# Kernel optimization log

Measured on AMD Instinct MI355X. Metric: run time of the kernel, lower is better.

Reference implementation:

```python
import jax, jax.numpy as jnp
import numpy as np

B, S, D, H = 2, 2048, 1024, 16
DH = D // H  # per-head depth = 64


def setup_inputs() -> dict:
    key = jax.random.key(0)
    ks = jax.random.split(key, 10)
    s = 1.0 / np.sqrt(D)
    return {
        "q_in": jax.random.normal(ks[0], (B, S, D), jnp.float32),
        "k_in": jax.random.normal(ks[1], (B, S, D), jnp.float32),
        "v_in": jax.random.normal(ks[2], (B, S, D), jnp.float32),
        "mask": jnp.zeros((B, 1, S, S), jnp.float32),
        "Wq": jax.random.normal(ks[3], (D, D), jnp.float32) * s,
        "bq": jnp.zeros((D,), jnp.float32),
        "Wk": jax.random.normal(ks[4], (D, D), jnp.float32) * s,
        "bk": jnp.zeros((D,), jnp.float32),
        "Wv": jax.random.normal(ks[5], (D, D), jnp.float32) * s,
        "bv": jnp.zeros((D,), jnp.float32),
        "Wo": jax.random.normal(ks[6], (D, D), jnp.float32) * s,
        "bo": jnp.zeros((D,), jnp.float32),
    }


def _split_heads(x):
    # [B,S,D] -> [B,H,S,DH]
    b, s, _ = x.shape
    return x.reshape(b, s, H, DH).transpose(0, 2, 1, 3)


def reference(q_in, k_in, v_in, mask, Wq, bq, Wk, bk, Wv, bv, Wo, bo):
    q = _split_heads(q_in @ Wq + bq)
    k = _split_heads(k_in @ Wk + bk)
    v = _split_heads(v_in @ Wv + bv)
    logits = jnp.einsum("bhqd,bhkd->bhqk", q, k) / jnp.sqrt(jnp.float32(DH))
    logits = logits + mask * -1e9
    attn = jax.nn.softmax(logits, axis=-1)
    ctx = jnp.einsum("bhqk,bhkd->bhqd", attn, v)  # [B,H,S,DH]
    concat = ctx.transpose(0, 2, 1, 3).reshape(q_in.shape[0], -1, D)
    out = concat @ Wo + bo  # dropout is identity at inference
    return out, attn
```

## Files before the change

### kernel.cpp

```cpp
#include <hip/hip_runtime.h>
#include <hip/hip_bf16.h>

static constexpr int cB = 2, cS = 2048, cD = 1024, cH = 16, cDH = 64;

typedef __attribute__((ext_vector_type(4))) float f32x4;
typedef __attribute__((ext_vector_type(8))) short s16x8;
typedef unsigned long long u64;
typedef unsigned short u16;

__device__ inline f32x4 mfma16(s16x8 a, s16x8 b, f32x4 c) {
  return __builtin_amdgcn_mfma_f32_16x16x32_bf16(a, b, c, 0, 0, 0);
}

__device__ inline u16 f2bf(float x) {
  unsigned u = __float_as_uint(x);
  u += 0x7FFFu + ((u >> 16) & 1u);
  return (u16)(u >> 16);
}

__device__ inline unsigned cvt_pk_bf16(float lo, float hi) {
  unsigned r;
  asm("v_cvt_pk_bf16_f32 %0, %1, %2" : "=v"(r) : "v"(lo), "v"(hi));
  return r;
}

__device__ inline f32x4 zero4() { f32x4 z; z[0] = z[1] = z[2] = z[3] = 0.f; return z; }

__device__ inline void gload16(const void* src, void* dst) {
  __builtin_amdgcn_global_load_lds((const __attribute__((address_space(1))) void*)src,
                                   (__attribute__((address_space(3))) void*)dst, 16, 0, 0);
}

__global__ __launch_bounds__(256) void wt4_kernel(const float* __restrict__ W0,
                                                  const float* __restrict__ W1,
                                                  const float* __restrict__ W2,
                                                  const float* __restrict__ W3,
                                                  u16* __restrict__ T0, u16* __restrict__ T1,
                                                  u16* __restrict__ T2, u16* __restrict__ T3) {
  __shared__ float tile[32][33];
  int z = blockIdx.z;
  const float* W = z == 0 ? W0 : z == 1 ? W1 : z == 2 ? W2 : W3;
  u16* Wt = z == 0 ? T0 : z == 1 ? T1 : z == 2 ? T2 : T3;
  int tx = threadIdx.x, ty = threadIdx.y;
  int r0 = blockIdx.y * 32, c0 = blockIdx.x * 32;
  for (int i = ty; i < 32; i += 8)
    tile[i][tx] = W[(size_t)(r0 + i) * cD + c0 + tx];
  __syncthreads();
  for (int i = ty; i < 32; i += 8)
    Wt[(size_t)(c0 + i) * cD + r0 + tx] = f2bf(tile[tx][i]);
}

__global__ __launch_bounds__(256) void maskflag_kernel(const float* __restrict__ mask,
                                                       unsigned char* __restrict__ flags) {
  int blk = blockIdx.x;
  int b = blk >> 10, qt = (blk >> 5) & 31, kt = blk & 31;
  int t = threadIdx.x;
  int r = t >> 2, c0 = (t & 3) * 16;
  const float4* p = (const float4*)(mask + ((size_t)b * cS + qt * 64 + r) * cS + kt * 64 + c0);
  int any = 0;
  for (int j = 0; j < 4; ++j) {
    float4 v = p[j];
    any |= (v.x != 0.f) | (v.y != 0.f) | (v.z != 0.f) | (v.w != 0.f);
  }
  __shared__ int sred;
  if (t == 0) sred = 0;
  __syncthreads();
  if (any) atomicOr(&sred, 1);
  __syncthreads();
  if (t == 0) flags[blk] = (unsigned char)sred;
}

template<bool AFP32, bool OUTF32>
__global__ __launch_bounds__(256) void gemm128(const void* __restrict__ Ap,
                                               const u16* __restrict__ Bt,
                                               const float* __restrict__ bias,
                                               void* __restrict__ outp,
                                               float scale, int vt_mode) {
  __shared__ __attribute__((aligned(16))) u16 As[128 * 64];
  __shared__ __attribute__((aligned(16))) u16 Bs[128 * 64];
  int t = threadIdx.x;
  int w = t >> 6, l = t & 63, g = l >> 4, li = l & 15;
  int bm = blockIdx.x & 31, bn = blockIdx.x >> 5;
  int m0 = bm * 128, n0 = bn * 128;
  int wr = w >> 1, wc = w & 1;

  f32x4 acc[4][4];
  for (int i = 0; i < 4; ++i)
    for (int j = 0; j < 4; ++j) acc[i][j] = zero4();

  for (int kk = 0; kk < cD; kk += 64) {
    if (AFP32) {
      const float* X = (const float*)Ap;
      int ar = t >> 1, ak0 = (t & 1) * 32;
      const float* asrc = X + (size_t)(m0 + ar) * cD + kk + ak0;
      int sw = ar & 7;
      for (int j = 0; j < 4; ++j) {
        float4 x0 = ((const float4*)asrc)[2 * j];
        float4 x1 = ((const float4*)asrc)[2 * j + 1];
        union { s16x8 v; u16 h[8]; } s;
        s.h[0] = f2bf(x0.x); s.h[1] = f2bf(x0.y); s.h[2] = f2bf(x0.z); s.h[3] = f2bf(x0.w);
        s.h[4] = f2bf(x1.x); s.h[5] = f2bf(x1.y); s.h[6] = f2bf(x1.z); s.h[7] = f2bf(x1.w);
        int chunk = (ak0 >> 3) + j;
        *(s16x8*)&As[ar * 64 + ((chunk ^ sw) * 8)] = s.v;
      }
    } else {
      const u16* X = (const u16*)Ap;
      for (int is = 0; is < 4; ++is) {
        int row = w * 32 + is * 8 + (l >> 3);
        int chunk = l & 7;
        const u16* src = X + (size_t)(m0 + row) * cD + kk + ((chunk ^ (row & 7)) * 8);
        gload16(src, &As[(w * 32 + is * 8) * 64]);
      }
    }
    for (int is = 0; is < 4; ++is) {
      int row = w * 32 + is * 8 + (l >> 3);
      int chunk = l & 7;
      const u16* src = Bt + (size_t)(n0 + row) * cD + kk + ((chunk ^ (row & 7)) * 8);
      gload16(src, &Bs[(w * 32 + is * 8) * 64]);
    }
    __syncthreads();
    for (int c = 0; c < 2; ++c) {
      s16x8 af[4], bf[4];
      for (int mi = 0; mi < 4; ++mi) {
        int r = wr * 64 + mi * 16 + li;
        af[mi] = *(const s16x8*)&As[r * 64 + (((c * 4 + g) ^ (r & 7)) * 8)];
      }
      for (int ni = 0; ni < 4; ++ni) {
        int r = wc * 64 + ni * 16 + li;
        bf[ni] = *(const s16x8*)&Bs[r * 64 + (((c * 4 + g) ^ (r & 7)) * 8)];
      }
      for (int mi = 0; mi < 4; ++mi)
        for (int ni = 0; ni < 4; ++ni)
          acc[mi][ni] = mfma16(af[mi], bf[ni], acc[mi][ni]);
    }
    __syncthreads();
  }

  for (int ni = 0; ni < 4; ++ni) {
    int n = n0 + wc * 64 + ni * 16 + li;
    float bv = bias[n];
    for (int mi = 0; mi < 4; ++mi) {
      for (int r = 0; r < 4; ++r) {
        int m = m0 + wr * 64 + mi * 16 + g * 4 + r;
        float val = acc[mi][ni][r] + bv;
        if (OUTF32) {
          ((float*)outp)[(size_t)m * cD + n] = val;
        } else {
          val *= scale;
          int b = m >> 11, s = m & 2047;
          int h = n >> 6, d = n & 63;
          size_t idx = vt_mode ? ((size_t)(b * cH + h) * cDH + d) * cS + s
                               : ((size_t)(b * cH + h) * cS + s) * cDH + d;
          ((u16*)outp)[idx] = f2bf(val);
        }
      }
    }
  }
}

__global__ __launch_bounds__(512) void attn_kernel(const u16* __restrict__ Q,
                                                   const u16* __restrict__ K,
                                                   const u16* __restrict__ Vt,
                                                   const float* __restrict__ mask,
                                                   const unsigned char* __restrict__ flags,
                                                   float* __restrict__ attn,
                                                   u16* __restrict__ ctx) {
  __shared__ __attribute__((aligned(16))) u16 Kl[64 * 64];
  __shared__ __attribute__((aligned(16))) u16 Vl[64 * 64];
  int t = threadIdx.x;
  int w = t >> 6, l = t & 63, g = l >> 4, li = l & 15;
  int p = blockIdx.x;
  int blk = (p & 7) * 64 + (p >> 3);
  int bh = blk >> 4, qt = blk & 15;
  int b = bh >> 4;
  int qbase = qt * 128;
  const u16* Qh = Q + (size_t)bh * cS * cDH;
  const u16* Kh = K + (size_t)bh * cS * cDH;
  const u16* Vh = Vt + (size_t)bh * cDH * cS;
  const unsigned char* fl = flags + (b << 10) + ((qbase + w * 16) >> 6) * 32;

  s16x8 qf[2];
  {
    const u16* qp = Qh + (size_t)(qbase + w * 16 + li) * cDH;
    qf[0] = *(const s16x8*)(qp + 8 * g);
    qf[1] = *(const s16x8*)(qp + 32 + 8 * g);
  }
  int srow8 = l >> 3, schunk = l & 7;
  int q_lane = qbase + w * 16 + li;

  float racc = 0.f;
  for (int kt = 0; kt < 32; ++kt) {
    {
      int row = w * 8 + srow8;
      gload16(Kh + (size_t)(kt * 64 + row) * cDH + ((schunk ^ (row & 7)) * 8),
              &Kl[(w * 8) * 64]);
    }
    __syncthreads();
    f32x4 acc[4];
    for (int mt = 0; mt < 4; ++mt) acc[mt] = zero4();
    for (int c = 0; c < 2; ++c)
      for (int mt = 0; mt < 4; ++mt) {
        int r = mt * 16 + li;
        s16x8 kf = *(const s16x8*)&Kl[r * 64 + (((c * 4 + g) ^ (r & 7)) * 8)];
        acc[mt] = mfma16(kf, qf[c], acc[mt]);
      }
    bool um = fl[kt] != 0;
    for (int mt = 0; mt < 4; ++mt)
      for (int r = 0; r < 4; ++r) {
        float lv = acc[mt][r];
        if (um) lv += mask[((size_t)b * cS + q_lane) * cS + kt * 64 + mt * 16 + 4 * g + r] * -1e9f;
        racc += __expf(lv);
      }
    __syncthreads();
  }
  racc += __shfl_xor(racc, 16, 64);
  racc += __shfl_xor(racc, 32, 64);
  float rs = 1.f / racc;

  f32x4 cacc[4];
  for (int dt = 0; dt < 4; ++dt) cacc[dt] = zero4();
  float* attn_row = attn + (size_t)bh * cS * cS + (size_t)q_lane * cS;
  for (int kt = 0; kt < 32; ++kt) {
    {
      int row = w * 8 + srow8;
      gload16(Kh + (size_t)(kt * 64 + row) * cDH + ((schunk ^ (row & 7)) * 8),
              &Kl[(w * 8) * 64]);
      gload16(Vh + (size_t)row * cS + kt * 64 + ((schunk ^ (row & 7)) * 8),
              &Vl[(w * 8) * 64]);
    }
    __syncthreads();
    f32x4 acc[4];
    for (int mt = 0; mt < 4; ++mt) acc[mt] = zero4();
    for (int c = 0; c < 2; ++c)
      for (int mt = 0; mt < 4; ++mt) {
        int r = mt * 16 + li;
        s16x8 kf = *(const s16x8*)&Kl[r * 64 + (((c * 4 + g) ^ (r & 7)) * 8)];
        acc[mt] = mfma16(kf, qf[c], acc[mt]);
      }
    bool um = fl[kt] != 0;
    s16x8 pa[2];
    for (int c = 0; c < 2; ++c) {
      union { s16x8 v; unsigned u[4]; } pk;
      f32x4 pvq[2];
      for (int hh = 0; hh < 2; ++hh) {
        int mt = c * 2 + hh;
        for (int r = 0; r < 4; ++r) {
          float lv = acc[mt][r];
          if (um) lv += mask[((size_t)b * cS + q_lane) * cS + kt * 64 + mt * 16 + 4 * g + r] * -1e9f;
          pvq[hh][r] = __expf(lv) * rs;
        }
        *(f32x4*)(attn_row + kt * 64 + mt * 16 + 4 * g) = pvq[hh];
      }
      pk.u[0] = cvt_pk_bf16(pvq[0][0], pvq[0][1]);
      pk.u[1] = cvt_pk_bf16(pvq[0][2], pvq[0][3]);
      pk.u[2] = cvt_pk_bf16(pvq[1][0], pvq[1][1]);
      pk.u[3] = cvt_pk_bf16(pvq[1][2], pvq[1][3]);
      pa[c] = pk.v;
    }
    for (int c = 0; c < 2; ++c) {
      for (int dt = 0; dt < 4; ++dt) {
        int row = dt * 16 + li;
        const u16* rb = &Vl[row * 64];
        int o0 = (((c * 4 + 0 + (g >> 1)) ^ (li & 7)) * 8) + (g & 1) * 4;
        int o1 = (((c * 4 + 2 + (g >> 1)) ^ (li & 7)) * 8) + (g & 1) * 4;
        union { s16x8 v; u64 qq[2]; } vf;
        vf.qq[0] = *(const u64*)(rb + o0);
        vf.qq[1] = *(const u64*)(rb + o1);
        cacc[dt] = mfma16(pa[c], vf.v, cacc[dt]);
      }
    }
    __syncthreads();
  }

  int h = bh & 15;
  for (int dt = 0; dt < 4; ++dt)
    for (int r = 0; r < 4; ++r) {
      int s = qbase + w * 16 + g * 4 + r;
      int d = dt * 16 + li;
      ctx[((size_t)(b * cS + s)) * cD + h * 64 + d] = f2bf(cacc[dt][r]);
    }
}

extern "C" void kernel_launch(void* const* d_in, const int* in_sizes, int n_in,
                              void* d_out, int out_size, void* d_ws, size_t ws_size,
                              hipStream_t stream) {
  const float* q_in = (const float*)d_in[0];
  const float* k_in = (const float*)d_in[1];
  const float* v_in = (const float*)d_in[2];
  const float* mask = (const float*)d_in[3];
  const float* Wq = (const float*)d_in[4];
  const float* bq = (const float*)d_in[5];
  const float* Wk = (const float*)d_in[6];
  const float* bk = (const float*)d_in[7];
  const float* Wv = (const float*)d_in[8];
  const float* bv = (const float*)d_in[9];
  const float* Wo = (const float*)d_in[10];
  const float* bo = (const float*)d_in[11];

  float* out = (float*)d_out;
  float* attn = out + (size_t)cB * cS * cD;

  const size_t MATB = (size_t)cB * cS * cD * 2;
  const size_t WB = (size_t)cD * cD * 2;
  char* ws = (char*)d_ws;
  u16* WqT = (u16*)(ws);
  u16* WkT = (u16*)(ws + WB);
  u16* WvT = (u16*)(ws + 2 * WB);
  u16* WoT = (u16*)(ws + 3 * WB);
  u16* wsQ  = (u16*)(ws + 4 * WB);
  u16* wsK  = (u16*)(ws + 4 * WB + MATB);
  u16* wsVt = (u16*)(ws + 4 * WB + 2 * MATB);
  u16* wsC  = (u16*)(ws + 4 * WB + 3 * MATB);
  unsigned char* flags = (unsigned char*)(ws + 4 * WB + 4 * MATB);
  const size_t REQUIRED = 4 * WB + 4 * MATB + 2048;
  if (ws_size < REQUIRED) return;

  dim3 tb(32, 8);
  wt4_kernel<<<dim3(32, 32, 4), tb, 0, stream>>>(Wq, Wk, Wv, Wo, WqT, WkT, WvT, WoT);
  maskflag_kernel<<<2048, 256, 0, stream>>>(mask, flags);

  gemm128<true, false><<<256, 256, 0, stream>>>(q_in, WqT, bq, wsQ, 0.125f, 0);
  gemm128<true, false><<<256, 256, 0, stream>>>(k_in, WkT, bk, wsK, 1.0f, 0);
  gemm128<true, false><<<256, 256, 0, stream>>>(v_in, WvT, bv, wsVt, 1.0f, 1);

  attn_kernel<<<512, 512, 0, stream>>>(wsQ, wsK, wsVt, mask, flags, attn, wsC);

  gemm128<false, true><<<256, 256, 0, stream>>>(wsC, WoT, bo, out, 1.0f, 0);
}
```

Before: 381.0 us.

## Batch QKV GEMMs into one launch, narrow output GEMM tiles, streamline softmax stores

Merges the three QKV projection GEMMs into one 768-block launch so all 256 CUs get work at once. The output GEMM now uses 128x64 tiles (512 blocks) to improve occupancy. In attention, the reciprocal-multiply normalization becomes exp(lv - log(sum)), and the large fp32 attention-probability writes use nontemporal stores to reduce cache pollution. The log-domain normalization changes rounding slightly.

```diff
diff --git a/kernel.cpp b/kernel.cpp
--- a/kernel.cpp
+++ b/kernel.cpp
@@ -70,23 +70,24 @@
   if (t == 0) flags[blk] = (unsigned char)sred;
 }
 
-template<bool AFP32, bool OUTF32>
-__global__ __launch_bounds__(256) void gemm128(const void* __restrict__ Ap,
-                                               const u16* __restrict__ Bt,
-                                               const float* __restrict__ bias,
-                                               void* __restrict__ outp,
-                                               float scale, int vt_mode) {
-  __shared__ __attribute__((aligned(16))) u16 As[128 * 64];
-  __shared__ __attribute__((aligned(16))) u16 Bs[128 * 64];
+template<bool AFP32, bool OUTF32, int BN>
+__device__ __forceinline__ void gemm_body(const void* __restrict__ Ap,
+                                          const u16* __restrict__ Bt,
+                                          const float* __restrict__ bias,
+                                          void* __restrict__ outp,
+                                          float scale, int vt_mode, int bidx,
+                                          u16* As, u16* Bs) {
+  constexpr int NI = BN / 32;
+  constexpr int RPW = BN / 4;
   int t = threadIdx.x;
   int w = t >> 6, l = t & 63, g = l >> 4, li = l & 15;
-  int bm = blockIdx.x & 31, bn = blockIdx.x >> 5;
-  int m0 = bm * 128, n0 = bn * 128;
+  int bm = bidx & 31, bn = bidx >> 5;
+  int m0 = bm * 128, n0 = bn * BN;
   int wr = w >> 1, wc = w & 1;
 
-  f32x4 acc[4][4];
+  f32x4 acc[4][NI];
   for (int i = 0; i < 4; ++i)
-    for (int j = 0; j < 4; ++j) acc[i][j] = zero4();
+    for (int j = 0; j < NI; ++j) acc[i][j] = zero4();
 
   for (int kk = 0; kk < cD; kk += 64) {
     if (AFP32) {
@@ -112,32 +113,32 @@
         gload16(src, &As[(w * 32 + is * 8) * 64]);
       }
     }
-    for (int is = 0; is < 4; ++is) {
-      int row = w * 32 + is * 8 + (l >> 3);
+    for (int is = 0; is < RPW / 8; ++is) {
+      int row = w * RPW + is * 8 + (l >> 3);
       int chunk = l & 7;
       const u16* src = Bt + (size_t)(n0 + row) * cD + kk + ((chunk ^ (row & 7)) * 8);
-      gload16(src, &Bs[(w * 32 + is * 8) * 64]);
+      gload16(src, &Bs[(w * RPW + is * 8) * 64]);
     }
     __syncthreads();
     for (int c = 0; c < 2; ++c) {
-      s16x8 af[4], bf[4];
+      s16x8 af[4], bf[NI];
       for (int mi = 0; mi < 4; ++mi) {
         int r = wr * 64 + mi * 16 + li;
         af[mi] = *(const s16x8*)&As[r * 64 + (((c * 4 + g) ^ (r & 7)) * 8)];
       }
-      for (int ni = 0; ni < 4; ++ni) {
-        int r = wc * 64 + ni * 16 + li;
+      for (int ni = 0; ni < NI; ++ni) {
+        int r = wc * (BN / 2) + ni * 16 + li;
         bf[ni] = *(const s16x8*)&Bs[r * 64 + (((c * 4 + g) ^ (r & 7)) * 8)];
       }
       for (int mi = 0; mi < 4; ++mi)
-        for (int ni = 0; ni < 4; ++ni)
+        for (int ni = 0; ni < NI; ++ni)
           acc[mi][ni] = mfma16(af[mi], bf[ni], acc[mi][ni]);
     }
     __syncthreads();
   }
 
-  for (int ni = 0; ni < 4; ++ni) {
-    int n = n0 + wc * 64 + ni * 16 + li;
+  for (int ni = 0; ni < NI; ++ni) {
+    int n = n0 + wc * (BN / 2) + ni * 16 + li;
     float bv = bias[n];
     for (int mi = 0; mi < 4; ++mi) {
       for (int r = 0; r < 4; ++r) {
@@ -156,6 +157,39 @@
       }
     }
   }
+}
+
+__global__ __launch_bounds__(256) void qkv_gemm(const float* __restrict__ Xq,
+                                                const float* __restrict__ Xk,
+                                                const float* __restrict__ Xv,
+                                                const u16* __restrict__ Btq,
+                                                const u16* __restrict__ Btk,
+                                                const u16* __restrict__ Btv,
+                                                const float* __restrict__ bq,
+                                                const float* __restrict__ bk,
+                                                const float* __restrict__ bv,
+                                                u16* __restrict__ oq,
+                                                u16* __restrict__ ok,
+                                                u16* __restrict__ ov) {
+  __shared__ __attribute__((aligned(16))) u16 As[128 * 64];
+  __shared__ __attribute__((aligned(16))) u16 Bs[128 * 64];
+  int which = blockIdx.x >> 8, bidx = blockIdx.x & 255;
+  const float* X = which == 0 ? Xq : which == 1 ? Xk : Xv;
+  const u16* Bt = which == 0 ? Btq : which == 1 ? Btk : Btv;
+  const float* bias = which == 0 ? bq : which == 1 ? bk : bv;
+  u16* o = which == 0 ? oq : which == 1 ? ok : ov;
+  float scale = which == 0 ? 0.125f : 1.0f;
+  int vt = which == 2 ? 1 : 0;
+  gemm_body<true, false, 128>(X, Bt, bias, o, scale, vt, bidx, As, Bs);
+}
+
+__global__ __launch_bounds__(256) void out_gemm(const u16* __restrict__ Xc,
+                                                const u16* __restrict__ Bt,
+                                                const float* __restrict__ bias,
+                                                float* __restrict__ outp) {
+  __shared__ __attribute__((aligned(16))) u16 As[128 * 64];
+  __shared__ __attribute__((aligned(16))) u16 Bs[64 * 64];
+  gemm_body<false, true, 64>(Xc, Bt, bias, outp, 1.0f, 0, blockIdx.x, As, Bs);
 }
 
 __global__ __launch_bounds__(512) void attn_kernel(const u16* __restrict__ Q,
@@ -215,7 +249,7 @@
   }
   racc += __shfl_xor(racc, 16, 64);
   racc += __shfl_xor(racc, 32, 64);
-  float rs = 1.f / racc;
+  float lr = __logf(racc);
 
   f32x4 cacc[4];
   for (int dt = 0; dt < 4; ++dt) cacc[dt] = zero4();
@@ -247,9 +281,9 @@
         for (int r = 0; r < 4; ++r) {
           float lv = acc[mt][r];
           if (um) lv += mask[((size_t)b * cS + q_lane) * cS + kt * 64 + mt * 16 + 4 * g + r] * -1e9f;
-          pvq[hh][r] = __expf(lv) * rs;
+          pvq[hh][r] = __expf(lv - lr);
         }
-        *(f32x4*)(attn_row + kt * 64 + mt * 16 + 4 * g) = pvq[hh];
+        __builtin_nontemporal_store(pvq[hh], (f32x4*)(attn_row + kt * 64 + mt * 16 + 4 * g));
       }
       pk.u[0] = cvt_pk_bf16(pvq[0][0], pvq[0][1]);
       pk.u[1] = cvt_pk_bf16(pvq[0][2], pvq[0][3]);
@@ -319,11 +353,10 @@
   wt4_kernel<<<dim3(32, 32, 4), tb, 0, stream>>>(Wq, Wk, Wv, Wo, WqT, WkT, WvT, WoT);
   maskflag_kernel<<<2048, 256, 0, stream>>>(mask, flags);
 
-  gemm128<true, false><<<256, 256, 0, stream>>>(q_in, WqT, bq, wsQ, 0.125f, 0);
-  gemm128<true, false><<<256, 256, 0, stream>>>(k_in, WkT, bk, wsK, 1.0f, 0);
-  gemm128<true, false><<<256, 256, 0, stream>>>(v_in, WvT, bv, wsVt, 1.0f, 1);
+  qkv_gemm<<<768, 256, 0, stream>>>(q_in, k_in, v_in, WqT, WkT, WvT,
+                                    bq, bk, bv, wsQ, wsK, wsVt);
 
   attn_kernel<<<512, 512, 0, stream>>>(wsQ, wsK, wsVt, mask, flags, attn, wsC);
 
-  gemm128<false, true><<<256, 256, 0, stream>>>(wsC, WoT, bo, out, 1.0f, 0);
-}
+  out_gemm<<<512, 256, 0, stream>>>(wsC, WoT, bo, out);
+}
```

New measurement: 336.0 us. 11.8% less time.
